# Kernel tuning notes

Hardware: AMD Instinct MI355X
Metric: run time of the kernel (lower is better)

## Reference

```python
import jax, jax.numpy as jnp
import numpy as np
from jax import lax

DN = ('NCHW', 'OIHW', 'NCHW')

def conv(x, w, b, stride=1):
    y = lax.conv_general_dilated(x, w, window_strides=(stride, stride),
                                 padding='VALID', dimension_numbers=DN)
    return y + b[None, :, None, None]

def maxpool(x, k=3, s=2):
    return lax.reduce_window(x, -jnp.inf, lax.max,
                             (1, 1, k, k), (1, 1, s, s), 'VALID')

def setup_inputs() -> dict:
    key = jax.random.key(0)
    ks = jax.random.split(key, 7)
    B = 2048
    x = jax.random.normal(ks[0], (B, 1, 28, 28), dtype=jnp.float32)
    w1 = jax.random.normal(ks[1], (64, 1, 3, 3), dtype=jnp.float32)
    b1 = jax.random.normal(ks[2], (64,), dtype=jnp.float32)
    w2 = jax.random.normal(ks[3], (64, 64, 3, 3), dtype=jnp.float32)
    b2 = jax.random.normal(ks[4], (64,), dtype=jnp.float32)
    w3 = jax.random.normal(ks[5], (10, 64, 4, 4), dtype=jnp.float32)
    b3 = jax.random.normal(ks[6], (10,), dtype=jnp.float32)
    return {"x": x, "w1": w1, "b1": b1, "w2": w2, "b2": b2, "w3": w3, "b3": b3}

def reference(x, w1, b1, w2, b2, w3, b3):
    h = conv(x, w1, b1)            # [B,64,26,26]
    h = maxpool(h)                 # [B,64,12,12]
    h = jnp.maximum(h, 0.0)
    h = conv(h, w2, b2)            # [B,64,10,10]
    h = maxpool(h)                 # [B,64,4,4]
    h = jnp.maximum(h, 0.0)
    h = conv(h, w3, b3)            # [B,10,1,1]
    return h.reshape(h.shape[0], -1)  # [B,10]
```

## Files before the change

kernel.cpp:

```cpp
#include <hip/hip_runtime.h>


typedef __attribute__((ext_vector_type(8))) short short8;
typedef __attribute__((ext_vector_type(4))) float f32x4;

__device__ inline short f2bf(float f) {
    union { float f; unsigned u; } v; v.f = f;
    unsigned r = (v.u + 0x7FFFu + ((v.u >> 16) & 1u)) >> 16;
    return (short)r;
}

__global__ __launch_bounds__(256) void convnet_fused(
    const float* __restrict__ x,
    const float* __restrict__ w1,
    const float* __restrict__ b1,
    const float* __restrict__ w2,
    const float* __restrict__ b2,
    const float* __restrict__ w3,
    const float* __restrict__ b3,
    float* __restrict__ out)
{
    __shared__ float lds_f[7424];
    short* h1t  = (short*)lds_f;
    float* img  = lds_f + 5184;
    float* cbuf = lds_f;
    float* h2t  = lds_f + 6400;
    float* prt  = lds_f;

    const int n_img = blockIdx.x;
    const int t = threadIdx.x;
    const int c = t >> 2;
    const int q = t & 3;

    const float* img_g = x + (size_t)n_img * 784;
    for (int i = t; i < 784; i += 256) img[i] = img_g[i];
    __syncthreads();

    {
        const int oy = (q >> 1) * 6, ox = (q & 1) * 6;
        const int iy0 = 2 * oy, ix0 = 2 * ox;
        float w[9];
        #pragma unroll
        for (int k = 0; k < 9; ++k) w[k] = w1[c * 9 + k];
        const float bias = b1[c];

        float rows[3][16];
        {
            const float* s0 = img + iy0 * 28 + ix0;
            const float* s1 = img + (iy0 + 1) * 28 + ix0;
            #pragma unroll
            for (int m = 0; m < 4; ++m) {
                *(float4*)(rows[0] + 4 * m) = *(const float4*)(s0 + 4 * m);
                *(float4*)(rows[1] + 4 * m) = *(const float4*)(s1 + 4 * m);
            }
        }
        float cm[3][6];

        #pragma unroll
        for (int r = 0; r < 13; ++r) {
            {
                const float* s2 = img + (iy0 + r + 2) * 28 + ix0;
                float* dst = rows[(r + 2) % 3];
                #pragma unroll
                for (int m = 0; m < 4; ++m)
                    *(float4*)(dst + 4 * m) = *(const float4*)(s2 + 4 * m);
            }
            const float* r0 = rows[r % 3];
            const float* r1 = rows[(r + 1) % 3];
            const float* r2 = rows[(r + 2) % 3];
            #pragma unroll
            for (int px = 0; px < 6; ++px) cm[r % 3][px] = -1e30f;
            #pragma unroll
            for (int xx = 0; xx < 13; ++xx) {
                float a = bias;
                #pragma unroll
                for (int j = 0; j < 3; ++j) {
                    a += r0[xx + j] * w[j];
                    a += r1[xx + j] * w[3 + j];
                    a += r2[xx + j] * w[6 + j];
                }
                if ((xx & 1) == 0) {
                    if (xx >= 2 && xx <= 12) cm[r % 3][xx / 2 - 1] = fmaxf(cm[r % 3][xx / 2 - 1], a);
                    if (xx <= 10)            cm[r % 3][xx / 2]     = fmaxf(cm[r % 3][xx / 2], a);
                } else {
                    cm[r % 3][xx / 2] = fmaxf(cm[r % 3][xx / 2], a);
                }
            }
            if (r >= 2 && (r & 1) == 0) {
                const int py = r / 2 - 1;
                #pragma unroll
                for (int px = 0; px < 6; ++px) {
                    float m = fmaxf(fmaxf(cm[0][px], cm[1][px]), cm[2][px]);
                    h1t[((oy + py) * 12 + ox + px) * 72 + c] = f2bf(fmaxf(m, 0.0f));
                }
            }
        }
    }
    __syncthreads();

    const int wv = t >> 6, lane = t & 63;
    const int quad = lane >> 4, mrow = lane & 15;
    {
        int base_el[7];
        #pragma unroll
        for (int nt = 0; nt < 7; ++nt) {
            int n = nt * 16 + mrow; if (n > 99) n = 99;
            int y = n / 10, xx = n - y * 10;
            base_el[nt] = (y * 12 + xx) * 72;
        }
        f32x4 acc[7];
        #pragma unroll
        for (int nt = 0; nt < 7; ++nt) acc[nt] = (f32x4){0.f, 0.f, 0.f, 0.f};

        const int cout = wv * 16 + mrow;
        #pragma unroll
        for (int h = 0; h < 2; ++h) {
            const int c0 = h * 32 + quad * 8;
            const float* runp = w2 + cout * 576 + c0 * 9;
            short8 af[9];
            #pragma unroll
            for (int m = 0; m < 18; ++m) {
                const float4 v = *(const float4*)(runp + 4 * m);
                const int i0 = 4 * m;
                af[(i0 + 0) % 9][(i0 + 0) / 9] = f2bf(v.x);
                af[(i0 + 1) % 9][(i0 + 1) / 9] = f2bf(v.y);
                af[(i0 + 2) % 9][(i0 + 2) / 9] = f2bf(v.z);
                af[(i0 + 3) % 9][(i0 + 3) / 9] = f2bf(v.w);
            }
            #pragma unroll
            for (int s = 0; s < 9; ++s) {
                const int ky = s / 3, kx = s - ky * 3;
                const int boff = (ky * 12 + kx) * 72 + h * 32 + quad * 8;
                #pragma unroll
                for (int nt = 0; nt < 7; ++nt) {
                    const short8 b = *(const short8*)(h1t + base_el[nt] + boff);
                    acc[nt] = __builtin_amdgcn_mfma_f32_16x16x32_bf16(af[s], b, acc[nt], 0, 0, 0);
                }
            }
        }
        __syncthreads();
        #pragma unroll
        for (int nt = 0; nt < 7; ++nt) {
            const int n = nt * 16 + mrow;
            if (n < 100) {
                #pragma unroll
                for (int r = 0; r < 4; ++r) {
                    const int co = wv * 16 + quad * 4 + r;
                    cbuf[co * 100 + n] = acc[nt][r] + b2[co];
                }
            }
        }
    }
    __syncthreads();

    {
        const float* cb = cbuf + c * 100;
        #pragma unroll
        for (int k = 0; k < 4; ++k) {
            const int pos = q * 4 + k;
            const int py = pos >> 2, px = pos & 3;
            float m = -1e30f;
            #pragma unroll
            for (int a = 0; a < 3; ++a)
                #pragma unroll
                for (int b = 0; b < 3; ++b)
                    m = fmaxf(m, cb[(2 * py + a) * 10 + (2 * px + b)]);
            h2t[pos * 64 + c] = fmaxf(m, 0.0f);
        }
    }
    __syncthreads();

    if (t < 160) {
        const int o = t >> 4, l = t & 15;
        const float* w3o = w3 + o * 1024;
        float s = 0.0f;
        #pragma unroll
        for (int cc = 0; cc < 4; ++cc) {
            const int cin = l * 4 + cc;
            const float4 wv4a = *(const float4*)(w3o + cin * 16);
            const float4 wv4b = *(const float4*)(w3o + cin * 16 + 4);
            const float4 wv4c = *(const float4*)(w3o + cin * 16 + 8);
            const float4 wv4d = *(const float4*)(w3o + cin * 16 + 12);
            const float* hh = h2t + cin;
            s += hh[0*64] * wv4a.x + hh[1*64] * wv4a.y + hh[2*64] * wv4a.z + hh[3*64] * wv4a.w;
            s += hh[4*64] * wv4b.x + hh[5*64] * wv4b.y + hh[6*64] * wv4b.z + hh[7*64] * wv4b.w;
            s += hh[8*64] * wv4c.x + hh[9*64] * wv4c.y + hh[10*64] * wv4c.z + hh[11*64] * wv4c.w;
            s += hh[12*64] * wv4d.x + hh[13*64] * wv4d.y + hh[14*64] * wv4d.z + hh[15*64] * wv4d.w;
        }
        prt[t] = s;
    }
    __syncthreads();
    if (t < 10) {
        float s = b3[t];
        #pragma unroll
        for (int l = 0; l < 16; ++l) s += prt[t * 16 + l];
        out[(size_t)n_img * 10 + t] = s;
    }
}

extern "C" void kernel_launch(void* const* d_in, const int* in_sizes, int n_in,
                              void* d_out, int out_size, void* d_ws, size_t ws_size,
                              hipStream_t stream) {
    const float* x  = (const float*)d_in[0];
    const float* w1 = (const float*)d_in[1];
    const float* b1 = (const float*)d_in[2];
    const float* w2 = (const float*)d_in[3];
    const float* b2 = (const float*)d_in[4];
    const float* w3 = (const float*)d_in[5];
    const float* b3 = (const float*)d_in[6];
    float* out = (float*)d_out;

    const int B = in_sizes[0] / 784;
    convnet_fused<<<B, 256, 0, stream>>>(x, w1, b1, w2, b2, w3, b3, out);
}
```

Measured before the change: 135.8 us.

## Pre-convert w2 to bf16, use 32x32 MFMA, read image directly from global

Adds a prep kernel that converts w2 to bf16 in a [tap][cout][cin] layout held in workspace, so the fused kernel loads MFMA A fragments directly instead of converting per block. The conv2 GEMM moves from 16x16x32 to 32x32x16 MFMA tiles split across waves by M tile and N pair. The LDS image staging is dropped and conv1 reads the input from global. The cbuf row stride is padded to 101 to reduce bank conflicts, and the conv3 dot product is restructured to use vectorised LDS reads. The extra launch and the padded N tiles (128 columns for 100 outputs) add overhead, and the global image reads depend on cache hits.

```diff
diff --git a/kernel.cpp b/kernel.cpp
--- a/kernel.cpp
+++ b/kernel.cpp
@@ -2,7 +2,7 @@
 
 
 typedef __attribute__((ext_vector_type(8))) short short8;
-typedef __attribute__((ext_vector_type(4))) float f32x4;
+typedef __attribute__((ext_vector_type(16))) float f32x16;
 
 __device__ inline short f2bf(float f) {
     union { float f; unsigned u; } v; v.f = f;
@@ -10,21 +10,28 @@
     return (short)r;
 }
 
+__global__ __launch_bounds__(256) void prep_w2(const float* __restrict__ w2,
+                                               short* __restrict__ w2r) {
+    int i = blockIdx.x * 256 + threadIdx.x;
+    if (i >= 36864) return;
+    int s = i >> 12, cout = (i >> 6) & 63, cin = i & 63;
+    w2r[i] = f2bf(w2[cout * 576 + cin * 9 + s]);
+}
+
 __global__ __launch_bounds__(256) void convnet_fused(
     const float* __restrict__ x,
     const float* __restrict__ w1,
     const float* __restrict__ b1,
-    const float* __restrict__ w2,
+    const short* __restrict__ w2r,
     const float* __restrict__ b2,
     const float* __restrict__ w3,
     const float* __restrict__ b3,
     float* __restrict__ out)
 {
-    __shared__ float lds_f[7424];
+    __shared__ float lds_f[7488];
     short* h1t  = (short*)lds_f;
-    float* img  = lds_f + 5184;
     float* cbuf = lds_f;
-    float* h2t  = lds_f + 6400;
+    float* h2t  = lds_f + 6464;
     float* prt  = lds_f;
 
     const int n_img = blockIdx.x;
@@ -33,8 +40,6 @@
     const int q = t & 3;
 
     const float* img_g = x + (size_t)n_img * 784;
-    for (int i = t; i < 784; i += 256) img[i] = img_g[i];
-    __syncthreads();
 
     {
         const int oy = (q >> 1) * 6, ox = (q & 1) * 6;
@@ -46,8 +51,8 @@
 
         float rows[3][16];
         {
-            const float* s0 = img + iy0 * 28 + ix0;
-            const float* s1 = img + (iy0 + 1) * 28 + ix0;
+            const float* s0 = img_g + iy0 * 28 + ix0;
+            const float* s1 = img_g + (iy0 + 1) * 28 + ix0;
             #pragma unroll
             for (int m = 0; m < 4; ++m) {
                 *(float4*)(rows[0] + 4 * m) = *(const float4*)(s0 + 4 * m);
@@ -55,11 +60,10 @@
             }
         }
         float cm[3][6];
-
         #pragma unroll
         for (int r = 0; r < 13; ++r) {
             {
-                const float* s2 = img + (iy0 + r + 2) * 28 + ix0;
+                const float* s2 = img_g + (iy0 + r + 2) * 28 + ix0;
                 float* dst = rows[(r + 2) % 3];
                 #pragma unroll
                 for (int m = 0; m < 4; ++m)
@@ -99,54 +103,46 @@
     __syncthreads();
 
     const int wv = t >> 6, lane = t & 63;
-    const int quad = lane >> 4, mrow = lane & 15;
+    const int mtile = wv & 1, npair = wv >> 1;
+    const int col32 = lane & 31, khalf = lane >> 5;
     {
-        int base_el[7];
-        #pragma unroll
-        for (int nt = 0; nt < 7; ++nt) {
-            int n = nt * 16 + mrow; if (n > 99) n = 99;
+        int base_el[2];
+        #pragma unroll
+        for (int nt2 = 0; nt2 < 2; ++nt2) {
+            int n = (npair * 2 + nt2) * 32 + col32;
+            if (n > 99) n = 99;
             int y = n / 10, xx = n - y * 10;
-            base_el[nt] = (y * 12 + xx) * 72;
-        }
-        f32x4 acc[7];
-        #pragma unroll
-        for (int nt = 0; nt < 7; ++nt) acc[nt] = (f32x4){0.f, 0.f, 0.f, 0.f};
-
-        const int cout = wv * 16 + mrow;
-        #pragma unroll
-        for (int h = 0; h < 2; ++h) {
-            const int c0 = h * 32 + quad * 8;
-            const float* runp = w2 + cout * 576 + c0 * 9;
-            short8 af[9];
-            #pragma unroll
-            for (int m = 0; m < 18; ++m) {
-                const float4 v = *(const float4*)(runp + 4 * m);
-                const int i0 = 4 * m;
-                af[(i0 + 0) % 9][(i0 + 0) / 9] = f2bf(v.x);
-                af[(i0 + 1) % 9][(i0 + 1) / 9] = f2bf(v.y);
-                af[(i0 + 2) % 9][(i0 + 2) / 9] = f2bf(v.z);
-                af[(i0 + 3) % 9][(i0 + 3) / 9] = f2bf(v.w);
-            }
-            #pragma unroll
-            for (int s = 0; s < 9; ++s) {
-                const int ky = s / 3, kx = s - ky * 3;
-                const int boff = (ky * 12 + kx) * 72 + h * 32 + quad * 8;
-                #pragma unroll
-                for (int nt = 0; nt < 7; ++nt) {
-                    const short8 b = *(const short8*)(h1t + base_el[nt] + boff);
-                    acc[nt] = __builtin_amdgcn_mfma_f32_16x16x32_bf16(af[s], b, acc[nt], 0, 0, 0);
-                }
+            base_el[nt2] = (y * 12 + xx) * 72;
+        }
+        f32x16 acc[2];
+        #pragma unroll
+        for (int nt2 = 0; nt2 < 2; ++nt2)
+            #pragma unroll
+            for (int r = 0; r < 16; ++r) acc[nt2][r] = 0.0f;
+
+        #pragma unroll
+        for (int step = 0; step < 36; ++step) {
+            const int s = step >> 2;
+            const int cinb = (step & 3) * 16 + khalf * 8;
+            const short8 a = *(const short8*)(w2r + s * 4096 + (mtile * 32 + col32) * 64 + cinb);
+            const int ky = s / 3, kx = s - ky * 3;
+            const int toff = (ky * 12 + kx) * 72 + cinb;
+            #pragma unroll
+            for (int nt2 = 0; nt2 < 2; ++nt2) {
+                const short8 b = *(const short8*)(h1t + base_el[nt2] + toff);
+                acc[nt2] = __builtin_amdgcn_mfma_f32_32x32x16_bf16(a, b, acc[nt2], 0, 0, 0);
             }
         }
         __syncthreads();
         #pragma unroll
-        for (int nt = 0; nt < 7; ++nt) {
-            const int n = nt * 16 + mrow;
+        for (int nt2 = 0; nt2 < 2; ++nt2) {
+            const int n = (npair * 2 + nt2) * 32 + col32;
             if (n < 100) {
                 #pragma unroll
-                for (int r = 0; r < 4; ++r) {
-                    const int co = wv * 16 + quad * 4 + r;
-                    cbuf[co * 100 + n] = acc[nt][r] + b2[co];
+                for (int reg = 0; reg < 16; ++reg) {
+                    const int row = (reg & 3) + 8 * (reg >> 2) + 4 * khalf;
+                    const int cout = mtile * 32 + row;
+                    cbuf[cout * 101 + n] = acc[nt2][reg] + b2[cout];
                 }
             }
         }
@@ -154,7 +150,7 @@
     __syncthreads();
 
     {
-        const float* cb = cbuf + c * 100;
+        const float* cb = cbuf + c * 101;
         #pragma unroll
         for (int k = 0; k < 4; ++k) {
             const int pos = q * 4 + k;
@@ -171,21 +167,19 @@
     __syncthreads();
 
     if (t < 160) {
-        const int o = t >> 4, l = t & 15;
-        const float* w3o = w3 + o * 1024;
+        const int o = t >> 4, g = t & 15;
+        const float* w3o = w3 + o * 1024 + g * 64;
+        float wr[4][16];
+        #pragma unroll
+        for (int cc = 0; cc < 4; ++cc)
+            #pragma unroll
+            for (int m = 0; m < 4; ++m)
+                *(float4*)(wr[cc] + 4 * m) = *(const float4*)(w3o + cc * 16 + 4 * m);
         float s = 0.0f;
         #pragma unroll
-        for (int cc = 0; cc < 4; ++cc) {
-            const int cin = l * 4 + cc;
-            const float4 wv4a = *(const float4*)(w3o + cin * 16);
-            const float4 wv4b = *(const float4*)(w3o + cin * 16 + 4);
-            const float4 wv4c = *(const float4*)(w3o + cin * 16 + 8);
-            const float4 wv4d = *(const float4*)(w3o + cin * 16 + 12);
-            const float* hh = h2t + cin;
-            s += hh[0*64] * wv4a.x + hh[1*64] * wv4a.y + hh[2*64] * wv4a.z + hh[3*64] * wv4a.w;
-            s += hh[4*64] * wv4b.x + hh[5*64] * wv4b.y + hh[6*64] * wv4b.z + hh[7*64] * wv4b.w;
-            s += hh[8*64] * wv4c.x + hh[9*64] * wv4c.y + hh[10*64] * wv4c.z + hh[11*64] * wv4c.w;
-            s += hh[12*64] * wv4d.x + hh[13*64] * wv4d.y + hh[14*64] * wv4d.z + hh[15*64] * wv4d.w;
+        for (int pos = 0; pos < 16; ++pos) {
+            const float4 hv = *(const float4*)(h2t + pos * 64 + g * 4);
+            s += hv.x * wr[0][pos] + hv.y * wr[1][pos] + hv.z * wr[2][pos] + hv.w * wr[3][pos];
         }
         prt[t] = s;
     }
@@ -193,7 +187,7 @@
     if (t < 10) {
         float s = b3[t];
         #pragma unroll
-        for (int l = 0; l < 16; ++l) s += prt[t * 16 + l];
+        for (int g = 0; g < 16; ++g) s += prt[t * 16 + g];
         out[(size_t)n_img * 10 + t] = s;
     }
 }
@@ -209,7 +203,9 @@
     const float* w3 = (const float*)d_in[5];
     const float* b3 = (const float*)d_in[6];
     float* out = (float*)d_out;
+    short* w2r = (short*)d_ws;
 
     const int B = in_sizes[0] / 784;
-    convnet_fused<<<B, 256, 0, stream>>>(x, w1, b1, w2, b2, w3, b3, out);
-}
+    prep_w2<<<144, 256, 0, stream>>>(w2, w2r);
+    convnet_fused<<<B, 256, 0, stream>>>(x, w1, b1, w2r, b2, w3, b3, out);
+}
```

Result: faster. 130.5 us (-3.9%).
